# Kernel optimization log

Hardware: AMD Instinct MI355X
Metric: run time of the kernel (lower is better)

## Reference

```python
import jax, jax.numpy as jnp
import numpy as np

B, S, FEA, T = 32, 8, 2560, 800   # batch, speakers, feature dim (20*128), time frames
N_CLUSTERS, EMB = 512, 256        # speaker-embedding dictionary shape (m)
H = 8                             # n_heads


def setup_inputs() -> dict:
    key = jax.random.key(0)
    ks = jax.random.split(key, 9)
    x = jax.random.normal(ks[0], (B, FEA, T), dtype=jnp.float32)
    mask = jax.random.uniform(ks[1], (B, S, T), dtype=jnp.float32)
    # learned params
    W_w = jax.random.normal(ks[2], (H, FEA), dtype=jnp.float32) * 0.02
    W_b = jnp.zeros((H,), dtype=jnp.float32)
    U_w = jax.random.normal(ks[3], (H, EMB), dtype=jnp.float32) * 0.02
    U_b = jnp.zeros((H,), dtype=jnp.float32)
    v_w = jax.random.normal(ks[4], (1, H), dtype=jnp.float32) * 0.1
    v_b = jnp.zeros((1,), dtype=jnp.float32)
    # speaker-embedding dictionary (self.m loaded from .npy)
    m = jax.random.normal(ks[5], (N_CLUSTERS, EMB), dtype=jnp.float32)
    return {"x": x, "mask": mask, "W_w": W_w, "W_b": W_b,
            "U_w": U_w, "U_b": U_b, "v_w": v_w, "v_b": v_b, "m": m}


def reference(x, mask, W_w, W_b, U_w, U_b, v_w, v_b, m):
    # masked mean-pool over time: (B,S,Fea) -- avoids the torch .repeat blowup
    pooled = jnp.einsum('bft,bst->bsf', x, mask)
    denom = jnp.sum(mask, axis=2)[..., None] + 1e-10   # (B,S,1)
    x2 = pooled / denom                                 # (B,S,Fea)
    # additive attention scores over clusters
    w = x2 @ W_w.T + W_b                                # (B,S,H)
    u = m @ U_w.T + U_b                                 # (N,H)
    s = jnp.tanh(w[:, :, None, :] + u[None, None, :, :])  # (B,S,N,H)
    c = jnp.einsum('bsnh,h->bsn', s, v_w[0]) + v_b[0]   # (B,S,N)
    a = jax.nn.sigmoid(c)
    # gated weighted sum of cluster embeddings
    e = jnp.einsum('bsn,ne->bse', a, m)                 # (B,S,Emb)
    return e
```

## Files before the change

kernel.cpp:

```cpp
#include <hip/hip_runtime.h>
#include <hip/hip_bf16.h>
#include <math.h>

#define B 32
#define S 8
#define FEA 2560
#define T 800
#define NCL 512
#define EMB 256
#define H 8

#define BF 64
#define SEC 128
#define NSEC 6
#define MROWB 1664

typedef __attribute__((ext_vector_type(8))) short bf16x8;
typedef __attribute__((ext_vector_type(4))) float f32x4;

__device__ __forceinline__ short4 cvt_bf16x4(float4 v) {
    union { short4 s4; __hip_bfloat162 h[2]; } u;
    u.h[0] = __float22bfloat162_rn(make_float2(v.x, v.y));
    u.h[1] = __float22bfloat162_rn(make_float2(v.z, v.w));
    return u.s4;
}

#define LOAD_SEC(s) {                                                               \
    _Pragma("unroll")                                                               \
    for (int r = 0; r < 8; ++r)                                                     \
        R[r] = *(const float4*)(xb + (size_t)(f0 + r * 8 + (tid >> 5)) * T          \
                                + (s) * SEC + (tid & 31) * 4);                      \
}

#define WRITE_SEC() {                                                               \
    _Pragma("unroll")                                                               \
    for (int r = 0; r < 8; ++r) {                                                   \
        const int row_ = r * 8 + (tid >> 5);                                        \
        *(short4*)(xls + row_ * 256 + (((tid & 31) * 8) ^ ((row_ & 7) << 4)))       \
            = cvt_bf16x4(R[r]);                                                     \
    }                                                                               \
}

#define CSTEP(sec, st) {                                                            \
    const bf16x8 bx_ = *(const bf16x8*)(xls + xrow * 256                            \
                          + ((((st) & 3) * 64 + kb16) ^ xswz));                     \
    const bf16x8 am_ = *(const bf16x8*)((const char*)mask_l + mbase                 \
                          + ((((sec) * 4 + (st)) * 64 + kb16) ^ mswz));             \
    acc = __builtin_amdgcn_mfma_f32_16x16x32_bf16(am_, bx_, acc, 0, 0, 0);          \
}

#define CSEC(sec) { CSTEP(sec,0) CSTEP(sec,1) CSTEP(sec,2) CSTEP(sec,3) }

__global__ __launch_bounds__(256, 5) void pool_kernel(const float* __restrict__ x,
                                                      const float* __restrict__ mask,
                                                      float* __restrict__ pooled) {
    const int b = blockIdx.y;

    __shared__ short mask_l[S * (MROWB / 2)];
    __shared__ char  xls[16384];

    const int tid = threadIdx.x;
    const int f0  = blockIdx.x * BF;
    const float* xb = x + (size_t)b * FEA * T;

    float4 R[8];

    LOAD_SEC(0)

    for (int v = tid; v < S * 200; v += 256) {
        const int s = v / 200, c4 = v % 200;
        const float4 mv = *(const float4*)(mask + ((size_t)(b * S + s)) * T + c4 * 4);
        const int byte = s * MROWB + ((c4 * 8) ^ (s << 4));
        *(short4*)((char*)mask_l + byte) = cvt_bf16x4(mv);
    }

    WRITE_SEC()
    LOAD_SEC(1)
    __syncthreads();

    const int wave = tid >> 6, lane = tid & 63;
    const int kb16 = (lane >> 4) * 16;
    const int xrow = wave * 16 + (lane & 15);
    const int xswz = (xrow & 7) << 4;
    const int srow = lane & 7;
    const int mbase = srow * MROWB;
    const int mswz = srow << 4;

    f32x4 acc = {0.f, 0.f, 0.f, 0.f};

    #pragma unroll 1
    for (int sec = 0; sec < NSEC; ++sec) {
        CSEC(sec)
        __syncthreads();
        if (sec < NSEC - 1) {
            WRITE_SEC()
            if (sec < NSEC - 2) LOAD_SEC(sec + 2)
        }
        __syncthreads();
    }

    {
        const float* xt = xb + (size_t)(f0 + xrow) * T + 768 + (lane >> 4) * 8;
        const float4 t0 = *(const float4*)(xt);
        const float4 t1 = *(const float4*)(xt + 4);
        union { bf16x8 v; short4 s4[2]; } Bx;
        Bx.s4[0] = cvt_bf16x4(t0);
        Bx.s4[1] = cvt_bf16x4(t1);
        const bf16x8 am = *(const bf16x8*)((const char*)mask_l + mbase
                              + ((24 * 64 + kb16) ^ mswz));
        acc = __builtin_amdgcn_mfma_f32_16x16x32_bf16(am, Bx.v, acc, 0, 0, 0);
    }

    if (lane < 32) {
        const int col = lane & 15;
        #pragma unroll
        for (int i = 0; i < 4; ++i) {
            const int sr = (lane >> 4) * 4 + i;
            pooled[(size_t)(b * S + sr) * FEA + f0 + wave * 16 + col] = acc[i];
        }
    }
}

__global__ __launch_bounds__(256) void wden_kernel(const float* __restrict__ pooled,
                                                   const float* __restrict__ mask,
                                                   const float* __restrict__ W_w,
                                                   const float* __restrict__ W_b,
                                                   const float* __restrict__ U_w,
                                                   const float* __restrict__ U_b,
                                                   const float* __restrict__ m,
                                                   float* __restrict__ w_out,
                                                   float* __restrict__ u_out,
                                                   float* __restrict__ out) {
    __shared__ float dred[4];
    __shared__ float wred[4][8];
    const int bs  = blockIdx.x;
    const int tid = threadIdx.x;
    const int lane = tid & 63, wave = tid >> 6;

    out[bs * EMB + tid] = 0.f;

    {
        const int job = tid >> 4, sub = tid & 15;
        const int cl  = 2 * bs + (job >> 3), h = job & 7;
        float pu = 0.f;
        #pragma unroll 4
        for (int e = sub; e < EMB; e += 16)
            pu += m[cl * EMB + e] * U_w[h * EMB + e];
        #pragma unroll
        for (int off = 8; off > 0; off >>= 1) pu += __shfl_xor(pu, off, 64);
        if (sub == 0) u_out[cl * H + h] = pu + U_b[h];
    }

    const float4* mk4 = (const float4*)(mask + (size_t)bs * T);
    float p = 0.f;
    if (tid < 200) {
        const float4 v = mk4[tid];
        p = v.x + v.y + v.z + v.w;
    }
    #pragma unroll
    for (int off = 32; off > 0; off >>= 1) p += __shfl_xor(p, off, 64);
    if (lane == 0) dred[wave] = p;
    __syncthreads();
    const float inv_d = 1.f / (dred[0] + dred[1] + dred[2] + dred[3] + 1e-10f);

    const float4* p4 = (const float4*)(pooled + (size_t)bs * FEA);
    const float4* W4 = (const float4*)W_w;
    float acc[8];
    #pragma unroll
    for (int h = 0; h < 8; ++h) acc[h] = 0.f;
    #pragma unroll 1
    for (int i = tid; i < FEA / 4; i += 256) {
        float4 xv = p4[i];
        xv.x *= inv_d; xv.y *= inv_d; xv.z *= inv_d; xv.w *= inv_d;
        #pragma unroll
        for (int h = 0; h < 8; ++h) {
            const float4 wv = W4[h * (FEA / 4) + i];
            acc[h] += xv.x * wv.x + xv.y * wv.y + xv.z * wv.z + xv.w * wv.w;
        }
    }
    #pragma unroll
    for (int h = 0; h < 8; ++h) {
        float v = acc[h];
        #pragma unroll
        for (int off = 32; off > 0; off >>= 1) v += __shfl_xor(v, off, 64);
        if (lane == 0) wred[wave][h] = v;
    }
    __syncthreads();
    if (tid < 8)
        w_out[bs * H + tid] = wred[0][tid] + wred[1][tid] + wred[2][tid] + wred[3][tid] + W_b[tid];
}

__global__ __launch_bounds__(256) void egemv_kernel(const float* __restrict__ w_buf,
                                                    const float* __restrict__ u_buf,
                                                    const float* __restrict__ v_w,
                                                    const float* __restrict__ v_b,
                                                    const float* __restrict__ m,
                                                    float* __restrict__ out) {
    __shared__ float a_sh[128];
    const int bs = blockIdx.x >> 2, q = blockIdx.x & 3;
    const int tid = threadIdx.x;
    const int n0 = q * 128;

    if (tid < 128) {
        const int n = n0 + tid;
        float c = v_b[0];
        #pragma unroll
        for (int h = 0; h < 8; ++h)
            c += tanhf(w_buf[bs * H + h] + u_buf[n * H + h]) * v_w[h];
        a_sh[tid] = 1.f / (1.f + expf(-c));
    }
    __syncthreads();

    float acc = 0.f;
    #pragma unroll 8
    for (int j = 0; j < 128; ++j)
        acc += a_sh[j] * m[(n0 + j) * EMB + tid];
    atomicAdd(&out[bs * EMB + tid], acc);
}

extern "C" void kernel_launch(void* const* d_in, const int* in_sizes, int n_in,
                              void* d_out, int out_size, void* d_ws, size_t ws_size,
                              hipStream_t stream) {
    const float* x    = (const float*)d_in[0];
    const float* mask = (const float*)d_in[1];
    const float* W_w  = (const float*)d_in[2];
    const float* W_b  = (const float*)d_in[3];
    const float* U_w  = (const float*)d_in[4];
    const float* U_b  = (const float*)d_in[5];
    const float* v_w  = (const float*)d_in[6];
    const float* v_b  = (const float*)d_in[7];
    const float* m    = (const float*)d_in[8];
    float* out = (float*)d_out;

    float* ws     = (float*)d_ws;
    float* pooled = ws;
    float* u_buf  = pooled + B * S * FEA;
    float* w_buf  = u_buf + NCL * H;

    pool_kernel<<<dim3(FEA / BF, B), 256, 0, stream>>>(x, mask, pooled);
    wden_kernel<<<B * S, 256, 0, stream>>>(pooled, mask, W_w, W_b, U_w, U_b, m,
                                           w_buf, u_buf, out);
    egemv_kernel<<<B * S * 4, 256, 0, stream>>>(w_buf, u_buf, v_w, v_b, m, out);
}
```

Before: 60.40 us.

## Restructure pooling kernel to stream contiguous 16-row tiles with double-buffered LDS

The pooling kernel now gives each block 10 tiles of 16 feature rows over the full time axis, loading each tile as a contiguous 51 KB chunk instead of strided 128-column sections. Tiles are double-buffered in LDS while the next tile is loaded from global memory, which is meant to make x reads fully sequential and cut redundant mask staging across blocks. Only wave 0 runs the MFMA chain; the other waves just move data. The grid shrinks from 1280 to 512 blocks, and the larger LDS footprint (about 64 KB per block) lowers occupancy.

```diff
diff --git a/kernel.cpp b/kernel.cpp
--- a/kernel.cpp
+++ b/kernel.cpp
@@ -10,10 +10,8 @@
 #define EMB 256
 #define H 8
 
-#define BF 64
-#define SEC 128
-#define NSEC 6
-#define MROWB 1664
+#define TPB 10
+#define XROWB 1600
 
 typedef __attribute__((ext_vector_type(8))) short bf16x8;
 typedef __attribute__((ext_vector_type(4))) float f32x4;
@@ -25,99 +23,88 @@
     return u.s4;
 }
 
-#define LOAD_SEC(s) {                                                               \
+#define LOAD_T(t) {                                                                 \
+    const float4* p_ = xb4 + (size_t)(tile0 + (t)) * 3200;                          \
     _Pragma("unroll")                                                               \
-    for (int r = 0; r < 8; ++r)                                                     \
-        R[r] = *(const float4*)(xb + (size_t)(f0 + r * 8 + (tid >> 5)) * T          \
-                                + (s) * SEC + (tid & 31) * 4);                      \
-}
-
-#define WRITE_SEC() {                                                               \
+    for (int i = 0; i < 13; ++i) {                                                  \
+        const int v = i * 256 + tid;                                                \
+        if (v < 3200) R[i] = p_[v];                                                 \
+    }                                                                               \
+}
+
+#define WRITE_T(bufsel) {                                                           \
+    char* dst_ = (char*)xl[bufsel];                                                 \
     _Pragma("unroll")                                                               \
-    for (int r = 0; r < 8; ++r) {                                                   \
-        const int row_ = r * 8 + (tid >> 5);                                        \
-        *(short4*)(xls + row_ * 256 + (((tid & 31) * 8) ^ ((row_ & 7) << 4)))       \
-            = cvt_bf16x4(R[r]);                                                     \
+    for (int i = 0; i < 13; ++i) {                                                  \
+        const int v = i * 256 + tid;                                                \
+        if (v < 3200) {                                                             \
+            const int row_ = v / 200, c4_ = v - row_ * 200;                         \
+            *(short4*)(dst_ + row_ * XROWB + ((c4_ * 8) ^ ((row_ & 7) << 4)))       \
+                = cvt_bf16x4(R[i]);                                                 \
+        }                                                                           \
     }                                                                               \
 }
 
-#define CSTEP(sec, st) {                                                            \
-    const bf16x8 bx_ = *(const bf16x8*)(xls + xrow * 256                            \
-                          + ((((st) & 3) * 64 + kb16) ^ xswz));                     \
-    const bf16x8 am_ = *(const bf16x8*)((const char*)mask_l + mbase                 \
-                          + ((((sec) * 4 + (st)) * 64 + kb16) ^ mswz));             \
-    acc = __builtin_amdgcn_mfma_f32_16x16x32_bf16(am_, bx_, acc, 0, 0, 0);          \
-}
-
-#define CSEC(sec) { CSTEP(sec,0) CSTEP(sec,1) CSTEP(sec,2) CSTEP(sec,3) }
-
-__global__ __launch_bounds__(256, 5) void pool_kernel(const float* __restrict__ x,
-                                                      const float* __restrict__ mask,
-                                                      float* __restrict__ pooled) {
-    const int b = blockIdx.y;
-
-    __shared__ short mask_l[S * (MROWB / 2)];
-    __shared__ char  xls[16384];
+__global__ __launch_bounds__(256) void pool_kernel(const float* __restrict__ x,
+                                                   const float* __restrict__ mask,
+                                                   float* __restrict__ pooled) {
+    const int b = blockIdx.y, fg = blockIdx.x;
+
+    __shared__ short mask_l[S * (XROWB / 2)];
+    __shared__ short xl[2][16 * (XROWB / 2)];
 
     const int tid = threadIdx.x;
-    const int f0  = blockIdx.x * BF;
-    const float* xb = x + (size_t)b * FEA * T;
-
-    float4 R[8];
-
-    LOAD_SEC(0)
+    const float4* xb4 = (const float4*)(x + (size_t)b * FEA * T);
+    const int tile0 = fg * TPB;
+
+    float4 R[13];
+
+    LOAD_T(0)
 
     for (int v = tid; v < S * 200; v += 256) {
         const int s = v / 200, c4 = v % 200;
         const float4 mv = *(const float4*)(mask + ((size_t)(b * S + s)) * T + c4 * 4);
-        const int byte = s * MROWB + ((c4 * 8) ^ (s << 4));
-        *(short4*)((char*)mask_l + byte) = cvt_bf16x4(mv);
-    }
-
-    WRITE_SEC()
-    LOAD_SEC(1)
-    __syncthreads();
-
-    const int wave = tid >> 6, lane = tid & 63;
+        *(short4*)((char*)mask_l + s * XROWB + ((c4 * 8) ^ (s << 4))) = cvt_bf16x4(mv);
+    }
+
+    WRITE_T(0)
+    LOAD_T(1)
+    __syncthreads();
+
+    const int lane = tid & 63, wave = tid >> 6;
     const int kb16 = (lane >> 4) * 16;
-    const int xrow = wave * 16 + (lane & 15);
+    const int xrow = lane & 15;
     const int xswz = (xrow & 7) << 4;
     const int srow = lane & 7;
-    const int mbase = srow * MROWB;
+    const int mbase = srow * XROWB;
     const int mswz = srow << 4;
 
-    f32x4 acc = {0.f, 0.f, 0.f, 0.f};
-
     #pragma unroll 1
-    for (int sec = 0; sec < NSEC; ++sec) {
-        CSEC(sec)
-        __syncthreads();
-        if (sec < NSEC - 1) {
-            WRITE_SEC()
-            if (sec < NSEC - 2) LOAD_SEC(sec + 2)
+    for (int t = 0; t < TPB; ++t) {
+        if (t < TPB - 1) WRITE_T((t + 1) & 1)
+        if (t < TPB - 2) LOAD_T(t + 2)
+        if (wave == 0) {
+            f32x4 acc = {0.f, 0.f, 0.f, 0.f};
+            const char* xbuf = (const char*)xl[t & 1];
+            #pragma unroll
+            for (int st = 0; st < 25; ++st) {
+                const bf16x8 bx = *(const bf16x8*)(xbuf + xrow * XROWB
+                                      + ((st * 64 + kb16) ^ xswz));
+                const bf16x8 am = *(const bf16x8*)((const char*)mask_l + mbase
+                                      + ((st * 64 + kb16) ^ mswz));
+                acc = __builtin_amdgcn_mfma_f32_16x16x32_bf16(am, bx, acc, 0, 0, 0);
+            }
+            if (lane < 32) {
+                const int col = lane & 15;
+                const int f0 = (tile0 + t) * 16;
+                #pragma unroll
+                for (int i = 0; i < 4; ++i) {
+                    const int sr = (lane >> 4) * 4 + i;
+                    pooled[(size_t)(b * S + sr) * FEA + f0 + col] = acc[i];
+                }
+            }
         }
         __syncthreads();
-    }
-
-    {
-        const float* xt = xb + (size_t)(f0 + xrow) * T + 768 + (lane >> 4) * 8;
-        const float4 t0 = *(const float4*)(xt);
-        const float4 t1 = *(const float4*)(xt + 4);
-        union { bf16x8 v; short4 s4[2]; } Bx;
-        Bx.s4[0] = cvt_bf16x4(t0);
-        Bx.s4[1] = cvt_bf16x4(t1);
-        const bf16x8 am = *(const bf16x8*)((const char*)mask_l + mbase
-                              + ((24 * 64 + kb16) ^ mswz));
-        acc = __builtin_amdgcn_mfma_f32_16x16x32_bf16(am, Bx.v, acc, 0, 0, 0);
-    }
-
-    if (lane < 32) {
-        const int col = lane & 15;
-        #pragma unroll
-        for (int i = 0; i < 4; ++i) {
-            const int sr = (lane >> 4) * 4 + i;
-            pooled[(size_t)(b * S + sr) * FEA + f0 + wave * 16 + col] = acc[i];
-        }
     }
 }
 
@@ -237,7 +224,7 @@
     float* u_buf  = pooled + B * S * FEA;
     float* w_buf  = u_buf + NCL * H;
 
-    pool_kernel<<<dim3(FEA / BF, B), 256, 0, stream>>>(x, mask, pooled);
+    pool_kernel<<<dim3(FEA / (16 * TPB), B), 256, 0, stream>>>(x, mask, pooled);
     wden_kernel<<<B * S, 256, 0, stream>>>(pooled, mask, W_w, W_b, U_w, U_b, m,
                                            w_buf, u_buf, out);
     egemv_kernel<<<B * S * 4, 256, 0, stream>>>(w_buf, u_buf, v_w, v_b, m, out);
```

New measurement: 62.13 us. 1.03x slower.
